# Kernel optimization log

Measured on AMD Instinct MI355X. Metric: run time of the kernel, lower is better.

Reference implementation:

```python
import jax, jax.numpy as jnp
import numpy as np

DIM, NCOND, K, NFLOWS, HID = 8, 16, 5, 2, 8
TB = 3.0                      # tail bound B
CMAX = NCOND + DIM - 1        # 23, max conditioning width (zero-padded)
MINW = MINH = MIND = 1e-3


def _fcnn(x, W1, b1, W2, b2, W3, b3):
    h = jnp.tanh(x @ W1.T + b1)
    h = jnp.tanh(h @ W2.T + b2)
    return h @ W3.T + b3


def _rqs_fwd(x, uw, uh, ud, tb):
    # x: [N]; uw, uh: [N, K] (already softmaxed+scaled by caller, re-softmaxed
    # here to match the original RQS implementation); ud: [N, K+1] (padded)
    nb = uw.shape[-1]
    widths = MINW + (1.0 - MINW * nb) * jax.nn.softmax(uw, axis=-1)
    cumw = jnp.pad(jnp.cumsum(widths, axis=-1), ((0, 0), (1, 0)))
    cumw = (2.0 * tb) * cumw - tb
    cumw = cumw.at[:, 0].set(-tb).at[:, -1].set(tb)
    widths = cumw[:, 1:] - cumw[:, :-1]
    heights = MINH + (1.0 - MINH * nb) * jax.nn.softmax(uh, axis=-1)
    cumh = jnp.pad(jnp.cumsum(heights, axis=-1), ((0, 0), (1, 0)))
    cumh = (2.0 * tb) * cumh - tb
    cumh = cumh.at[:, 0].set(-tb).at[:, -1].set(tb)
    heights = cumh[:, 1:] - cumh[:, :-1]
    derivs = MIND + jax.nn.softplus(ud)
    # searchsorted with eps on last edge
    idx = (jnp.sum(x[:, None] >= cumw.at[:, -1].add(1e-6), axis=-1) - 1)[:, None]
    take = lambda a: jnp.take_along_axis(a, idx, axis=-1)[:, 0]
    icw, ibw, ich, ih = take(cumw), take(widths), take(cumh), take(heights)
    idelta = take(heights / widths)
    d0, d1 = take(derivs), take(derivs[:, 1:])
    th = (x - icw) / ibw
    t2, tomt = th * th, th * (1.0 - th)
    den = idelta + (d0 + d1 - 2.0 * idelta) * tomt
    z = ich + ih * (idelta * t2 + d0 * tomt) / den
    ld = jnp.log(idelta ** 2 * (d1 * t2 + 2.0 * idelta * tomt + d0 * (1.0 - th) ** 2)) - 2.0 * jnp.log(den)
    return z, ld


def _unconstrained_rqs(x, W, H, D, tb):
    inside = (x >= -tb) & (x <= tb)
    const = float(np.log(np.exp(1.0 - MIND) - 1.0))
    Dp = jnp.pad(D, ((0, 0), (1, 1)), constant_values=const)
    z_in, ld_in = _rqs_fwd(jnp.clip(x, -tb, tb), W, H, Dp, tb)
    return jnp.where(inside, z_in, x), jnp.where(inside, ld_in, 0.0)


def setup_inputs() -> dict:
    key = jax.random.key(0)
    ks = jax.random.split(key, 16)
    N = 524288
    s = 0.3
    inp = {
        "x_inp": jax.random.normal(ks[0], (N, DIM), jnp.float32),
        "cond_inp": jax.random.normal(ks[1], (N, NCOND), jnp.float32),
        # init (base-dist) nets, one per dim; first layer zero-padded to CMAX
        "Wi1": s * jax.random.normal(ks[2], (DIM, HID, CMAX), jnp.float32),
        "bi1": s * jax.random.normal(ks[3], (DIM, HID), jnp.float32),
        "Wi2": s * jax.random.normal(ks[4], (DIM, HID, HID), jnp.float32),
        "bi2": s * jax.random.normal(ks[5], (DIM, HID), jnp.float32),
        "Wi3": s * jax.random.normal(ks[6], (DIM, 2, HID), jnp.float32),
        "bi3": s * jax.random.normal(ks[7], (DIM, 2), jnp.float32),
        # flow nets, per (dim, flow)
        "Wf1": s * jax.random.normal(ks[8], (DIM, NFLOWS, HID, CMAX), jnp.float32),
        "bf1": s * jax.random.normal(ks[9], (DIM, NFLOWS, HID), jnp.float32),
        "Wf2": s * jax.random.normal(ks[10], (DIM, NFLOWS, HID, HID), jnp.float32),
        "bf2": s * jax.random.normal(ks[11], (DIM, NFLOWS, HID), jnp.float32),
        "Wf3": s * jax.random.normal(ks[12], (DIM, NFLOWS, 3 * K - 1, HID), jnp.float32),
        "bf3": s * jax.random.normal(ks[13], (DIM, NFLOWS, 3 * K - 1), jnp.float32),
    }
    return inp


def reference(x_inp, cond_inp, Wi1, bi1, Wi2, bi2, Wi3, bi3,
              Wf1, bf1, Wf2, bf2, Wf3, bf3):
    N = x_inp.shape[0]
    logp_cols = []
    for jd in range(DIM):
        pad = jnp.zeros((N, CMAX - NCOND - jd), x_inp.dtype)
        cond_jd = jnp.concatenate([cond_inp, x_inp[:, :jd], pad], axis=1)  # [N, CMAX]
        # gumbel base-dist params
        outg = _fcnn(cond_jd, Wi1[jd], bi1[jd], Wi2[jd], bi2[jd], Wi3[jd], bi3[jd])
        mu, sig = outg[:, 0], jnp.exp(outg[:, 1])
        x = x_inp[:, jd]
        ld_sum = jnp.zeros((N,), x_inp.dtype)
        for jf in range(NFLOWS):
            out = _fcnn(cond_jd, Wf1[jd, jf], bf1[jd, jf], Wf2[jd, jf], bf2[jd, jf],
                        Wf3[jd, jf], bf3[jd, jf])  # [N, 3K-1]
            W = 2.0 * TB * jax.nn.softmax(out[:, :K], axis=1)
            H = 2.0 * TB * jax.nn.softmax(out[:, K:2 * K], axis=1)
            D = jax.nn.softplus(out[:, 2 * K:])
            x, ld = _unconstrained_rqs(x, W, H, D, TB)
            ld_sum = ld_sum + ld
        z = (x - mu) / sig
        lp = -(z + jnp.exp(-z)) - jnp.log(sig)  # Gumbel log_prob
        lp = jnp.where(jnp.isnan(lp) | jnp.isinf(lp), -100.0, lp)
        logp_cols.append(ld_sum + lp)
    return jnp.sum(jnp.stack(logp_cols, axis=1), axis=1)
```

## Files before the change

### kernel.cpp

```cpp
#include <hip/hip_runtime.h>
#include <math.h>

__device__ __forceinline__ float rcp_(float x) { return __fdividef(1.0f, x); }

__device__ __forceinline__ float tanh_(float x) {
    float t = x * x;
    float p = t + 378.0f;
    p = fmaf(p, t, 17325.0f);
    p = fmaf(p, t, 135135.0f);
    float q = fmaf(28.0f, t, 3150.0f);
    q = fmaf(q, t, 62370.0f);
    q = fmaf(q, t, 135135.0f);
    float r = (x * p) * rcp_(q);
    return fminf(fmaxf(r, -1.0f), 1.0f);
}

__device__ __forceinline__ float sp2_(float x) {
    return __logf(2.0f + __expf(x));
}

__device__ __forceinline__ void dsm5_(float o0, float o1, float o2, float o3, float o4,
                                      float* __restrict__ w) {
    float e0 = __expf(o0), e1 = __expf(o1), e2 = __expf(o2),
          e3 = __expf(o3), e4 = __expf(o4);
    float inv = 6.0f * rcp_(((e0 + e1) + (e2 + e3)) + e4);
    float f0 = __expf(e0 * inv);
    float f1 = __expf(e1 * inv);
    float f2 = __expf(e2 * inv);
    float f3 = __expf(e3 * inv);
    float f4 = __expf(e4 * inv);
    float t = 0.995f * rcp_(((f0 + f1) + (f2 + f3)) + f4);
    w[0] = fmaf(f0, t, 0.001f);
    w[1] = fmaf(f1, t, 0.001f);
    w[2] = fmaf(f2, t, 0.001f);
    w[3] = fmaf(f3, t, 0.001f);
    w[4] = fmaf(f4, t, 0.001f);
}

__global__ __launch_bounds__(512)
void zero_out(float* __restrict__ out, int n4) {
    int i = blockIdx.x * blockDim.x + threadIdx.x;
    if (i < n4) ((float4*)out)[i] = (float4){0.0f, 0.0f, 0.0f, 0.0f};
}

__global__ __launch_bounds__(512)
void nsf_kernel(const float* __restrict__ x_inp, const float* __restrict__ cond_inp,
                const float* __restrict__ Wi1, const float* __restrict__ bi1,
                const float* __restrict__ Wi2, const float* __restrict__ bi2,
                const float* __restrict__ Wi3, const float* __restrict__ bi3,
                const float* __restrict__ Wf1, const float* __restrict__ bf1,
                const float* __restrict__ Wf2, const float* __restrict__ bf2,
                const float* __restrict__ Wf3, const float* __restrict__ bf3,
                float* __restrict__ out, int N)
{
    const int jd = blockIdx.y;
    int s = blockIdx.x * 512 + threadIdx.x;
    int sl = (s < N) ? s : (N - 1);

    float cond[23];
    float xcur;
    {
        const float4* cp = (const float4*)(cond_inp + (size_t)sl * 16);
        float4 c0 = cp[0], c1 = cp[1], c2 = cp[2], c3 = cp[3];
        cond[0]=c0.x;  cond[1]=c0.y;  cond[2]=c0.z;  cond[3]=c0.w;
        cond[4]=c1.x;  cond[5]=c1.y;  cond[6]=c1.z;  cond[7]=c1.w;
        cond[8]=c2.x;  cond[9]=c2.y;  cond[10]=c2.z; cond[11]=c2.w;
        cond[12]=c3.x; cond[13]=c3.y; cond[14]=c3.z; cond[15]=c3.w;

        const float4* xp = (const float4*)(x_inp + (size_t)sl * 8);
        float4 a = xp[0], b = xp[1];
        float xv[8] = {a.x, a.y, a.z, a.w, b.x, b.y, b.z, b.w};
#pragma unroll
        for (int t = 0; t < 7; ++t)
            cond[16 + t] = (t < jd) ? xv[t] : 0.0f;
        xcur = xv[0];
#pragma unroll
        for (int t = 1; t < 8; ++t) xcur = (jd == t) ? xv[t] : xcur;
    }

    float g0, g1;
    {
        const float* W1 = Wi1 + (size_t)jd * 184;
        const float* b1 = bi1 + jd * 8;
        const float* W2 = Wi2 + (size_t)jd * 64;
        const float* b2 = bi2 + jd * 8;
        const float* W3 = Wi3 + (size_t)jd * 16;
        const float* b3 = bi3 + jd * 2;
        float h1[8], h2[8];
#pragma unroll
        for (int i = 0; i < 8; ++i) {
            float a = b1[i];
#pragma unroll
            for (int c = 0; c < 23; ++c) a = fmaf(W1[i * 23 + c], cond[c], a);
            h1[i] = tanh_(a);
        }
#pragma unroll
        for (int i = 0; i < 8; ++i) {
            float a = b2[i];
#pragma unroll
            for (int c = 0; c < 8; ++c) a = fmaf(W2[i * 8 + c], h1[c], a);
            h2[i] = tanh_(a);
        }
        g0 = b3[0]; g1 = b3[1];
#pragma unroll
        for (int c = 0; c < 8; ++c) {
            g0 = fmaf(W3[c], h2[c], g0);
            g1 = fmaf(W3[8 + c], h2[c], g1);
        }
    }

    float ldsum = 0.0f;
#pragma unroll
    for (int jf = 0; jf < 2; ++jf) {
        const int nf = jd * 2 + jf;
        const float* F1  = Wf1 + (size_t)nf * 184;
        const float* fb1 = bf1 + nf * 8;
        const float* F2  = Wf2 + (size_t)nf * 64;
        const float* fb2 = bf2 + nf * 8;
        const float* F3  = Wf3 + (size_t)nf * 112;
        const float* fb3 = bf3 + nf * 14;

        float h1[8], h2[8];
#pragma unroll
        for (int i = 0; i < 8; ++i) {
            float a = fb1[i];
#pragma unroll
            for (int c = 0; c < 23; ++c) a = fmaf(F1[i * 23 + c], cond[c], a);
            h1[i] = tanh_(a);
        }
#pragma unroll
        for (int i = 0; i < 8; ++i) {
            float a = fb2[i];
#pragma unroll
            for (int c = 0; c < 8; ++c) a = fmaf(F2[i * 8 + c], h1[c], a);
            h2[i] = tanh_(a);
        }
        float o[14];
#pragma unroll
        for (int i = 0; i < 14; ++i) {
            float a = fb3[i];
#pragma unroll
            for (int c = 0; c < 8; ++c) a = fmaf(F3[i * 8 + c], h2[c], a);
            o[i] = a;
        }

        float wv[5], hv[5];
        dsm5_(o[0], o[1], o[2], o[3], o[4], wv);
        dsm5_(o[5], o[6], o[7], o[8], o[9], hv);
        float di1 = sp2_(o[10]) + 0.001f;
        float di2 = sp2_(o[11]) + 0.001f;
        float di3 = sp2_(o[12]) + 0.001f;
        float di4 = sp2_(o[13]) + 0.001f;

        float xc = fminf(fmaxf(xcur, -3.0f), 3.0f);

        float runw = wv[0], runh = hv[0];
        float cwL = -3.0f, chL = -3.0f;
        float cwR = fmaf(6.0f, runw, -3.0f);
        float chR = fmaf(6.0f, runh, -3.0f);
        float icw = cwL, ibw = cwR - cwL, ich = chL, ihh = chR - chL;
        float d0 = 1.0f, d1 = di1;
#pragma unroll
        for (int k = 1; k < 5; ++k) {
            cwL = cwR; chL = chR;
            runw += wv[k]; runh += hv[k];
            cwR = (k == 4) ? 3.0f : fmaf(6.0f, runw, -3.0f);
            chR = (k == 4) ? 3.0f : fmaf(6.0f, runh, -3.0f);
            float dk0 = (k == 1) ? di1 : (k == 2) ? di2 : (k == 3) ? di3 : di4;
            float dk1 = (k == 1) ? di2 : (k == 2) ? di3 : (k == 3) ? di4 : 1.0f;
            bool sel = (xc >= cwL);
            icw = sel ? cwL : icw;
            ibw = sel ? (cwR - cwL) : ibw;
            ich = sel ? chL : ich;
            ihh = sel ? (chR - chL) : ihh;
            d0  = sel ? dk0 : d0;
            d1  = sel ? dk1 : d1;
        }

        float rb     = rcp_(ibw);
        float idelta = ihh * rb;
        float th     = (xc - icw) * rb;
        float t2     = th * th;
        float omt    = 1.0f - th;
        float tomt   = th * omt;
        float den    = fmaf(fmaf(-2.0f, idelta, d0 + d1), tomt, idelta);
        float rden   = rcp_(den);
        float xn     = fmaf(ihh * fmaf(idelta, t2, d0 * tomt), rden, ich);
        float num    = (idelta * idelta) *
                       fmaf(d1, t2, fmaf(idelta + idelta, tomt, d0 * (omt * omt)));
        float ldi    = __logf((num * rden) * rden);

        bool inside = (xcur >= -3.0f) && (xcur <= 3.0f);
        xcur  = inside ? xn : xcur;
        ldsum = inside ? (ldsum + ldi) : ldsum;
    }

    float z  = (xcur - g0) * __expf(-g1);
    float ez = __expf(-z);
    float lp = -(z + ez) - g1;
    if (isnan(lp) || isinf(lp)) lp = -100.0f;

    if (s < N) atomicAdd(&out[s], ldsum + lp);
}

extern "C" void kernel_launch(void* const* d_in, const int* in_sizes, int n_in,
                              void* d_out, int out_size, void* d_ws, size_t ws_size,
                              hipStream_t stream) {
    const float* x_inp    = (const float*)d_in[0];
    const float* cond_inp = (const float*)d_in[1];
    const float* Wi1 = (const float*)d_in[2];
    const float* bi1 = (const float*)d_in[3];
    const float* Wi2 = (const float*)d_in[4];
    const float* bi2 = (const float*)d_in[5];
    const float* Wi3 = (const float*)d_in[6];
    const float* bi3 = (const float*)d_in[7];
    const float* Wf1 = (const float*)d_in[8];
    const float* bf1 = (const float*)d_in[9];
    const float* Wf2 = (const float*)d_in[10];
    const float* bf2 = (const float*)d_in[11];
    const float* Wf3 = (const float*)d_in[12];
    const float* bf3 = (const float*)d_in[13];
    float* out = (float*)d_out;

    int N = out_size;
    int n4 = N / 4;
    hipLaunchKernelGGL(zero_out, dim3((n4 + 511) / 512), dim3(512), 0, stream, out, n4);

    dim3 grid((N + 511) / 512, 8, 1);
    hipLaunchKernelGGL(nsf_kernel, grid, dim3(512), 0, stream,
                       x_inp, cond_inp, Wi1, bi1, Wi2, bi2, Wi3, bi3,
                       Wf1, bf1, Wf2, bf2, Wf3, bf3, out, N);
}
```

Baseline: 268.2 us.

## Loop over all dimensions per thread and drop zero kernel and atomics

Each thread now loops over all 8 dimensions instead of using a grid y-dimension per dimension. The per-sample sum is kept in a register and written once, so the separate zero-fill kernel and the 8 atomic adds per output go away, and the cond/x inputs are loaded once rather than 8 times. In exchange the grid has 8x fewer threads, which lowers parallelism per launch (1024 blocks), and jd is now a runtime loop variable, so weight offsets and the cond/xcur selects are no longer specialized per block.

```diff
diff --git a/kernel.cpp b/kernel.cpp
--- a/kernel.cpp
+++ b/kernel.cpp
@@ -38,12 +38,6 @@
 }
 
 __global__ __launch_bounds__(512)
-void zero_out(float* __restrict__ out, int n4) {
-    int i = blockIdx.x * blockDim.x + threadIdx.x;
-    if (i < n4) ((float4*)out)[i] = (float4){0.0f, 0.0f, 0.0f, 0.0f};
-}
-
-__global__ __launch_bounds__(512)
 void nsf_kernel(const float* __restrict__ x_inp, const float* __restrict__ cond_inp,
                 const float* __restrict__ Wi1, const float* __restrict__ bi1,
                 const float* __restrict__ Wi2, const float* __restrict__ bi2,
@@ -53,154 +47,165 @@
                 const float* __restrict__ Wf3, const float* __restrict__ bf3,
                 float* __restrict__ out, int N)
 {
-    const int jd = blockIdx.y;
     int s = blockIdx.x * 512 + threadIdx.x;
     int sl = (s < N) ? s : (N - 1);
 
-    float cond[23];
-    float xcur;
+    float c16[16];
     {
         const float4* cp = (const float4*)(cond_inp + (size_t)sl * 16);
         float4 c0 = cp[0], c1 = cp[1], c2 = cp[2], c3 = cp[3];
-        cond[0]=c0.x;  cond[1]=c0.y;  cond[2]=c0.z;  cond[3]=c0.w;
-        cond[4]=c1.x;  cond[5]=c1.y;  cond[6]=c1.z;  cond[7]=c1.w;
-        cond[8]=c2.x;  cond[9]=c2.y;  cond[10]=c2.z; cond[11]=c2.w;
-        cond[12]=c3.x; cond[13]=c3.y; cond[14]=c3.z; cond[15]=c3.w;
-
+        c16[0]=c0.x;  c16[1]=c0.y;  c16[2]=c0.z;  c16[3]=c0.w;
+        c16[4]=c1.x;  c16[5]=c1.y;  c16[6]=c1.z;  c16[7]=c1.w;
+        c16[8]=c2.x;  c16[9]=c2.y;  c16[10]=c2.z; c16[11]=c2.w;
+        c16[12]=c3.x; c16[13]=c3.y; c16[14]=c3.z; c16[15]=c3.w;
+    }
+    float xv[8];
+    {
         const float4* xp = (const float4*)(x_inp + (size_t)sl * 8);
         float4 a = xp[0], b = xp[1];
-        float xv[8] = {a.x, a.y, a.z, a.w, b.x, b.y, b.z, b.w};
+        xv[0]=a.x; xv[1]=a.y; xv[2]=a.z; xv[3]=a.w;
+        xv[4]=b.x; xv[5]=b.y; xv[6]=b.z; xv[7]=b.w;
+    }
+
+    float total = 0.0f;
+
+#pragma unroll 1
+    for (int jd = 0; jd < 8; ++jd) {
+        float cond[23];
+#pragma unroll
+        for (int c = 0; c < 16; ++c) cond[c] = c16[c];
 #pragma unroll
         for (int t = 0; t < 7; ++t)
             cond[16 + t] = (t < jd) ? xv[t] : 0.0f;
-        xcur = xv[0];
+        float xcur = xv[0];
 #pragma unroll
         for (int t = 1; t < 8; ++t) xcur = (jd == t) ? xv[t] : xcur;
+
+        float g0, g1;
+        {
+            const float* W1 = Wi1 + (size_t)jd * 184;
+            const float* b1 = bi1 + jd * 8;
+            const float* W2 = Wi2 + (size_t)jd * 64;
+            const float* b2 = bi2 + jd * 8;
+            const float* W3 = Wi3 + (size_t)jd * 16;
+            const float* b3 = bi3 + jd * 2;
+            float h1[8], h2[8];
+#pragma unroll
+            for (int i = 0; i < 8; ++i) {
+                float a = b1[i];
+#pragma unroll
+                for (int c = 0; c < 23; ++c) a = fmaf(W1[i * 23 + c], cond[c], a);
+                h1[i] = tanh_(a);
+            }
+#pragma unroll
+            for (int i = 0; i < 8; ++i) {
+                float a = b2[i];
+#pragma unroll
+                for (int c = 0; c < 8; ++c) a = fmaf(W2[i * 8 + c], h1[c], a);
+                h2[i] = tanh_(a);
+            }
+            g0 = b3[0]; g1 = b3[1];
+#pragma unroll
+            for (int c = 0; c < 8; ++c) {
+                g0 = fmaf(W3[c], h2[c], g0);
+                g1 = fmaf(W3[8 + c], h2[c], g1);
+            }
+        }
+
+        float ldsum = 0.0f;
+#pragma unroll
+        for (int jf = 0; jf < 2; ++jf) {
+            const int nf = jd * 2 + jf;
+            const float* F1  = Wf1 + (size_t)nf * 184;
+            const float* fb1 = bf1 + nf * 8;
+            const float* F2  = Wf2 + (size_t)nf * 64;
+            const float* fb2 = bf2 + nf * 8;
+            const float* F3  = Wf3 + (size_t)nf * 112;
+            const float* fb3 = bf3 + nf * 14;
+
+            float h1[8], h2[8];
+#pragma unroll
+            for (int i = 0; i < 8; ++i) {
+                float a = fb1[i];
+#pragma unroll
+                for (int c = 0; c < 23; ++c) a = fmaf(F1[i * 23 + c], cond[c], a);
+                h1[i] = tanh_(a);
+            }
+#pragma unroll
+            for (int i = 0; i < 8; ++i) {
+                float a = fb2[i];
+#pragma unroll
+                for (int c = 0; c < 8; ++c) a = fmaf(F2[i * 8 + c], h1[c], a);
+                h2[i] = tanh_(a);
+            }
+            float o[14];
+#pragma unroll
+            for (int i = 0; i < 14; ++i) {
+                float a = fb3[i];
+#pragma unroll
+                for (int c = 0; c < 8; ++c) a = fmaf(F3[i * 8 + c], h2[c], a);
+                o[i] = a;
+            }
+
+            float wv[5], hv[5];
+            dsm5_(o[0], o[1], o[2], o[3], o[4], wv);
+            dsm5_(o[5], o[6], o[7], o[8], o[9], hv);
+            float di1 = sp2_(o[10]) + 0.001f;
+            float di2 = sp2_(o[11]) + 0.001f;
+            float di3 = sp2_(o[12]) + 0.001f;
+            float di4 = sp2_(o[13]) + 0.001f;
+
+            float xc = fminf(fmaxf(xcur, -3.0f), 3.0f);
+
+            float runw = wv[0], runh = hv[0];
+            float cwL = -3.0f, chL = -3.0f;
+            float cwR = fmaf(6.0f, runw, -3.0f);
+            float chR = fmaf(6.0f, runh, -3.0f);
+            float icw = cwL, ibw = cwR - cwL, ich = chL, ihh = chR - chL;
+            float d0 = 1.0f, d1 = di1;
+#pragma unroll
+            for (int k = 1; k < 5; ++k) {
+                cwL = cwR; chL = chR;
+                runw += wv[k]; runh += hv[k];
+                cwR = (k == 4) ? 3.0f : fmaf(6.0f, runw, -3.0f);
+                chR = (k == 4) ? 3.0f : fmaf(6.0f, runh, -3.0f);
+                float dk0 = (k == 1) ? di1 : (k == 2) ? di2 : (k == 3) ? di3 : di4;
+                float dk1 = (k == 1) ? di2 : (k == 2) ? di3 : (k == 3) ? di4 : 1.0f;
+                bool sel = (xc >= cwL);
+                icw = sel ? cwL : icw;
+                ibw = sel ? (cwR - cwL) : ibw;
+                ich = sel ? chL : ich;
+                ihh = sel ? (chR - chL) : ihh;
+                d0  = sel ? dk0 : d0;
+                d1  = sel ? dk1 : d1;
+            }
+
+            float rb     = rcp_(ibw);
+            float idelta = ihh * rb;
+            float th     = (xc - icw) * rb;
+            float t2     = th * th;
+            float omt    = 1.0f - th;
+            float tomt   = th * omt;
+            float den    = fmaf(fmaf(-2.0f, idelta, d0 + d1), tomt, idelta);
+            float rden   = rcp_(den);
+            float xn     = fmaf(ihh * fmaf(idelta, t2, d0 * tomt), rden, ich);
+            float num    = (idelta * idelta) *
+                           fmaf(d1, t2, fmaf(idelta + idelta, tomt, d0 * (omt * omt)));
+            float ldi    = __logf((num * rden) * rden);
+
+            bool inside = (xcur >= -3.0f) && (xcur <= 3.0f);
+            xcur  = inside ? xn : xcur;
+            ldsum = inside ? (ldsum + ldi) : ldsum;
+        }
+
+        float z  = (xcur - g0) * __expf(-g1);
+        float ez = __expf(-z);
+        float lp = -(z + ez) - g1;
+        if (isnan(lp) || isinf(lp)) lp = -100.0f;
+        total += ldsum + lp;
     }
 
-    float g0, g1;
-    {
-        const float* W1 = Wi1 + (size_t)jd * 184;
-        const float* b1 = bi1 + jd * 8;
-        const float* W2 = Wi2 + (size_t)jd * 64;
-        const float* b2 = bi2 + jd * 8;
-        const float* W3 = Wi3 + (size_t)jd * 16;
-        const float* b3 = bi3 + jd * 2;
-        float h1[8], h2[8];
-#pragma unroll
-        for (int i = 0; i < 8; ++i) {
-            float a = b1[i];
-#pragma unroll
-            for (int c = 0; c < 23; ++c) a = fmaf(W1[i * 23 + c], cond[c], a);
-            h1[i] = tanh_(a);
-        }
-#pragma unroll
-        for (int i = 0; i < 8; ++i) {
-            float a = b2[i];
-#pragma unroll
-            for (int c = 0; c < 8; ++c) a = fmaf(W2[i * 8 + c], h1[c], a);
-            h2[i] = tanh_(a);
-        }
-        g0 = b3[0]; g1 = b3[1];
-#pragma unroll
-        for (int c = 0; c < 8; ++c) {
-            g0 = fmaf(W3[c], h2[c], g0);
-            g1 = fmaf(W3[8 + c], h2[c], g1);
-        }
-    }
-
-    float ldsum = 0.0f;
-#pragma unroll
-    for (int jf = 0; jf < 2; ++jf) {
-        const int nf = jd * 2 + jf;
-        const float* F1  = Wf1 + (size_t)nf * 184;
-        const float* fb1 = bf1 + nf * 8;
-        const float* F2  = Wf2 + (size_t)nf * 64;
-        const float* fb2 = bf2 + nf * 8;
-        const float* F3  = Wf3 + (size_t)nf * 112;
-        const float* fb3 = bf3 + nf * 14;
-
-        float h1[8], h2[8];
-#pragma unroll
-        for (int i = 0; i < 8; ++i) {
-            float a = fb1[i];
-#pragma unroll
-            for (int c = 0; c < 23; ++c) a = fmaf(F1[i * 23 + c], cond[c], a);
-            h1[i] = tanh_(a);
-        }
-#pragma unroll
-        for (int i = 0; i < 8; ++i) {
-            float a = fb2[i];
-#pragma unroll
-            for (int c = 0; c < 8; ++c) a = fmaf(F2[i * 8 + c], h1[c], a);
-            h2[i] = tanh_(a);
-        }
-        float o[14];
-#pragma unroll
-        for (int i = 0; i < 14; ++i) {
-            float a = fb3[i];
-#pragma unroll
-            for (int c = 0; c < 8; ++c) a = fmaf(F3[i * 8 + c], h2[c], a);
-            o[i] = a;
-        }
-
-        float wv[5], hv[5];
-        dsm5_(o[0], o[1], o[2], o[3], o[4], wv);
-        dsm5_(o[5], o[6], o[7], o[8], o[9], hv);
-        float di1 = sp2_(o[10]) + 0.001f;
-        float di2 = sp2_(o[11]) + 0.001f;
-        float di3 = sp2_(o[12]) + 0.001f;
-        float di4 = sp2_(o[13]) + 0.001f;
-
-        float xc = fminf(fmaxf(xcur, -3.0f), 3.0f);
-
-        float runw = wv[0], runh = hv[0];
-        float cwL = -3.0f, chL = -3.0f;
-        float cwR = fmaf(6.0f, runw, -3.0f);
-        float chR = fmaf(6.0f, runh, -3.0f);
-        float icw = cwL, ibw = cwR - cwL, ich = chL, ihh = chR - chL;
-        float d0 = 1.0f, d1 = di1;
-#pragma unroll
-        for (int k = 1; k < 5; ++k) {
-            cwL = cwR; chL = chR;
-            runw += wv[k]; runh += hv[k];
-            cwR = (k == 4) ? 3.0f : fmaf(6.0f, runw, -3.0f);
-            chR = (k == 4) ? 3.0f : fmaf(6.0f, runh, -3.0f);
-            float dk0 = (k == 1) ? di1 : (k == 2) ? di2 : (k == 3) ? di3 : di4;
-            float dk1 = (k == 1) ? di2 : (k == 2) ? di3 : (k == 3) ? di4 : 1.0f;
-            bool sel = (xc >= cwL);
-            icw = sel ? cwL : icw;
-            ibw = sel ? (cwR - cwL) : ibw;
-            ich = sel ? chL : ich;
-            ihh = sel ? (chR - chL) : ihh;
-            d0  = sel ? dk0 : d0;
-            d1  = sel ? dk1 : d1;
-        }
-
-        float rb     = rcp_(ibw);
-        float idelta = ihh * rb;
-        float th     = (xc - icw) * rb;
-        float t2     = th * th;
-        float omt    = 1.0f - th;
-        float tomt   = th * omt;
-        float den    = fmaf(fmaf(-2.0f, idelta, d0 + d1), tomt, idelta);
-        float rden   = rcp_(den);
-        float xn     = fmaf(ihh * fmaf(idelta, t2, d0 * tomt), rden, ich);
-        float num    = (idelta * idelta) *
-                       fmaf(d1, t2, fmaf(idelta + idelta, tomt, d0 * (omt * omt)));
-        float ldi    = __logf((num * rden) * rden);
-
-        bool inside = (xcur >= -3.0f) && (xcur <= 3.0f);
-        xcur  = inside ? xn : xcur;
-        ldsum = inside ? (ldsum + ldi) : ldsum;
-    }
-
-    float z  = (xcur - g0) * __expf(-g1);
-    float ez = __expf(-z);
-    float lp = -(z + ez) - g1;
-    if (isnan(lp) || isinf(lp)) lp = -100.0f;
-
-    if (s < N) atomicAdd(&out[s], ldsum + lp);
+    if (s < N) out[s] = total;
 }
 
 extern "C" void kernel_launch(void* const* d_in, const int* in_sizes, int n_in,
@@ -223,11 +228,8 @@
     float* out = (float*)d_out;
 
     int N = out_size;
-    int n4 = N / 4;
-    hipLaunchKernelGGL(zero_out, dim3((n4 + 511) / 512), dim3(512), 0, stream, out, n4);
-
-    dim3 grid((N + 511) / 512, 8, 1);
-    hipLaunchKernelGGL(nsf_kernel, grid, dim3(512), 0, stream,
+    int grid = (N + 511) / 512;
+    hipLaunchKernelGGL(nsf_kernel, dim3(grid), dim3(512), 0, stream,
                        x_inp, cond_inp, Wi1, bi1, Wi2, bi2, Wi3, bi3,
                        Wf1, bf1, Wf2, bf2, Wf3, bf3, out, N);
 }
```

Result: no change. 270.9 us (+1.0%).
